# Kernel tuning notes

Measured on AMD Instinct MI355X. Metric: run time of the kernel, lower is better.

The kernel has to match this reference:

```python
import jax, jax.numpy as jnp
import numpy as np

SEQ_DIM = 256
PAIR_DIM = 128
N_HEADS = 8
HIDDEN = 32
B, L = 4, 512


def layer_norm(x, gamma, beta, eps=1e-5):
    mu = jnp.mean(x, axis=-1, keepdims=True)
    var = jnp.var(x, axis=-1, keepdims=True)
    return (x - mu) * jax.lax.rsqrt(var + eps) * gamma + beta


def setup_inputs() -> dict:
    key = jax.random.key(0)
    ks = jax.random.split(key, 12)
    d = N_HEADS * HIDDEN
    s = 0.02
    return {
        "seq": jax.random.normal(ks[0], (B, L, SEQ_DIM), jnp.float32),
        "pair": jax.random.normal(ks[1], (B, L, L, PAIR_DIM), jnp.float32),
        "ln_seq_g": jnp.ones((SEQ_DIM,), jnp.float32),
        "ln_seq_b": jnp.zeros((SEQ_DIM,), jnp.float32),
        "ln_pair_g": jnp.ones((PAIR_DIM,), jnp.float32),
        "ln_pair_b": jnp.zeros((PAIR_DIM,), jnp.float32),
        "W_b": jax.random.normal(ks[2], (PAIR_DIM, N_HEADS), jnp.float32) * s,
        "W_q": jax.random.normal(ks[3], (SEQ_DIM, d), jnp.float32) * s,
        "W_k": jax.random.normal(ks[4], (SEQ_DIM, d), jnp.float32) * s,
        "W_v": jax.random.normal(ks[5], (SEQ_DIM, d), jnp.float32) * s,
        "W_g": jax.random.normal(ks[6], (SEQ_DIM, d), jnp.float32) * s,
        "b_g": jnp.zeros((d,), jnp.float32),
        "W_o": jax.random.normal(ks[7], (d, SEQ_DIM), jnp.float32) * s,
        "b_o": jnp.zeros((SEQ_DIM,), jnp.float32),
    }


def reference(seq, pair, ln_seq_g, ln_seq_b, ln_pair_g, ln_pair_b,
              W_b, W_q, W_k, W_v, W_g, b_g, W_o, b_o):
    b, l, _ = seq.shape
    factor = 1.0 / np.sqrt(HIDDEN).astype(np.float32)
    s = layer_norm(seq, ln_seq_g, ln_seq_b)
    p = layer_norm(pair, ln_pair_g, ln_pair_b)
    Q = (s @ W_q).reshape(b, l, N_HEADS, HIDDEN)
    K = (s @ W_k).reshape(b, l, N_HEADS, HIDDEN)
    V = (s @ W_v).reshape(b, l, N_HEADS, HIDDEN)
    # pair bias: [b, i, j, n] -> [b, n, i, j]
    bias = jnp.einsum('bijp,pn->bnij', p, W_b)
    att = jnp.einsum('binh,bjnh->bnij', Q, K) * factor + bias
    att = jax.nn.softmax(att, axis=-1)
    gate = jax.nn.sigmoid(s @ W_g + b_g).reshape(b, l, N_HEADS, HIDDEN)
    out = jnp.einsum('bnij,bjnh->binh', att, V) * gate
    out = out.reshape(b, l, N_HEADS * HIDDEN)
    return out @ W_o + b_o
```

## Files before the change

kernel.cpp:

```cpp
#include <hip/hip_runtime.h>
#include <math.h>

#define OFF_Q    0
#define OFF_K    (524288)
#define OFF_V    (524288*2)
#define OFF_G    (524288*3)
#define OFF_PRE  (524288*4)
#define OFF_BIAS (524288*5)

template <int CTRL>
__device__ __forceinline__ float dpp_mov(float x) {
  return __int_as_float(__builtin_amdgcn_update_dpp(0, __float_as_int(x), CTRL, 0xF, 0xF, true));
}
template <int CTRL>
__device__ __forceinline__ float dpp_add(float x) { return x + dpp_mov<CTRL>(x); }
__device__ __forceinline__ float red16(float v) {
  v = dpp_add<0xB1>(v);
  v = dpp_add<0x4E>(v);
  v = dpp_add<0x141>(v);
  v = dpp_add<0x140>(v);
  return v;
}

#define SEL8(a, f, out) do { \
// ... 91 lines not shown
#pragma unroll 4
    for (int p = 0; p < 256; ++p) {
      float4 a  = *(const float4*)(ap + p*36);
      float4 bv = *(const float4*)(bp + p*256);
      a0.x = fmaf(a.x, bv.x, a0.x); a0.y = fmaf(a.x, bv.y, a0.y);
      a0.z = fmaf(a.x, bv.z, a0.z); a0.w = fmaf(a.x, bv.w, a0.w);
      a1.x = fmaf(a.y, bv.x, a1.x); a1.y = fmaf(a.y, bv.y, a1.y);
      a1.z = fmaf(a.y, bv.z, a1.z); a1.w = fmaf(a.y, bv.w, a1.w);
      a2.x = fmaf(a.z, bv.x, a2.x); a2.y = fmaf(a.z, bv.y, a2.y);
      a2.z = fmaf(a.z, bv.z, a2.z); a2.w = fmaf(a.z, bv.w, a2.w);
      a3.x = fmaf(a.w, bv.x, a3.x); a3.y = fmaf(a.w, bv.y, a3.y);
      a3.z = fmaf(a.w, bv.z, a3.z); a3.w = fmaf(a.w, bv.w, a3.w);
    }
    int mat = y >> 1;
    int col = cb + 4*cg2;
    float* outp = (mat == 0) ? Qw : (mat == 1) ? Kw : (mat == 2) ? Vw : Gw;
    if (mat == 0) {
      const float qs = 0.17677669529663687f;
      a0.x*=qs; a0.y*=qs; a0.z*=qs; a0.w*=qs;
      a1.x*=qs; a1.y*=qs; a1.z*=qs; a1.w*=qs;
      a2.x*=qs; a2.y*=qs; a2.z*=qs; a2.w*=qs;
      a3.x*=qs; a3.y*=qs; a3.z*=qs; a3.w*=qs;
    }
    if (mat == 3) {
      float4 g4 = *(const float4*)(bg + col);
      a0.x = 1.f/(1.f+__expf(-(a0.x+g4.x))); a0.y = 1.f/(1.f+__expf(-(a0.y+g4.y)));
      a0.z = 1.f/(1.f+__expf(-(a0.z+g4.z))); a0.w = 1.f/(1.f+__expf(-(a0.w+g4.w)));
      a1.x = 1.f/(1.f+__expf(-(a1.x+g4.x))); a1.y = 1.f/(1.f+__expf(-(a1.y+g4.y)));
      a1.z = 1.f/(1.f+__expf(-(a1.z+g4.z))); a1.w = 1.f/(1.f+__expf(-(a1.w+g4.w)));
      a2.x = 1.f/(1.f+__expf(-(a2.x+g4.x))); a2.y = 1.f/(1.f+__expf(-(a2.y+g4.y)));
      a2.z = 1.f/(1.f+__expf(-(a2.z+g4.z))); a2.w = 1.f/(1.f+__expf(-(a2.w+g4.w)));
      a3.x = 1.f/(1.f+__expf(-(a3.x+g4.x))); a3.y = 1.f/(1.f+__expf(-(a3.y+g4.y)));
      a3.z = 1.f/(1.f+__expf(-(a3.z+g4.z))); a3.w = 1.f/(1.f+__expf(-(a3.w+g4.w)));
    }
    int orow = m0 + 4*rg;
    *(float4*)(outp + (size_t)(orow+0)*256 + col) = a0;
    *(float4*)(outp + (size_t)(orow+1)*256 + col) = a1;
    *(float4*)(outp + (size_t)(orow+2)*256 + col) = a2;
    *(float4*)(outp + (size_t)(orow+3)*256 + col) = a3;
    return;
  }

  int bb2 = blk - 512;
  int b = bb2 >> 9, i = bb2 & 511;
  int lane = t & 63, w = t >> 6;
  int grp = lane >> 4, f = lane & 15;

  float wp[64];
  float cg[8] = {0,0,0,0,0,0,0,0}, cbv[8] = {0,0,0,0,0,0,0,0};
#pragma unroll
  for (int q = 0; q < 4; ++q) {
    int kA = 4*f + q, kB = 64 + 4*f + q;
    float gA = lpg[kA], bA = lpb[kA];
    float gB = lpg[kB], bB = lpb[kB];
    float4 uA0 = *(const float4*)(Wb + kA*8);
    float4 uA1 = *(const float4*)(Wb + kA*8 + 4);
    float4 uB0 = *(const float4*)(Wb + kB*8);
    float4 uB1 = *(const float4*)(Wb + kB*8 + 4);
    wp[q*8+0] = gA*uA0.x; cg[0] += wp[q*8+0]; cbv[0] = fmaf(bA, uA0.x, cbv[0]);
    wp[q*8+1] = gA*uA0.y; cg[1] += wp[q*8+1]; cbv[1] = fmaf(bA, uA0.y, cbv[1]);
    wp[q*8+2] = gA*uA0.z; cg[2] += wp[q*8+2]; cbv[2] = fmaf(bA, uA0.z, cbv[2]);
    wp[q*8+3] = gA*uA0.w; cg[3] += wp[q*8+3]; cbv[3] = fmaf(bA, uA0.w, cbv[3]);
    wp[q*8+4] = gA*uA1.x; cg[4] += wp[q*8+4]; cbv[4] = fmaf(bA, uA1.x, cbv[4]);
    wp[q*8+5] = gA*uA1.y; cg[5] += wp[q*8+5]; cbv[5] = fmaf(bA, uA1.y, cbv[5]);
    wp[q*8+6] = gA*uA1.z; cg[6] += wp[q*8+6]; cbv[6] = fmaf(bA, uA1.z, cbv[6]);
    wp[q*8+7] = gA*uA1.w; cg[7] += wp[q*8+7]; cbv[7] = fmaf(bA, uA1.w, cbv[7]);
    int qb8 = (4+q)*8;
    wp[qb8+0] = gB*uB0.x; cg[0] += wp[qb8+0]; cbv[0] = fmaf(bB, uB0.x, cbv[0]);
    wp[qb8+1] = gB*uB0.y; cg[1] += wp[qb8+1]; cbv[1] = fmaf(bB, uB0.y, cbv[1]);
    wp[qb8+2] = gB*uB0.z; cg[2] += wp[qb8+2]; cbv[2] = fmaf(bB, uB0.z, cbv[2]);
    wp[qb8+3] = gB*uB0.w; cg[3] += wp[qb8+3]; cbv[3] = fmaf(bB, uB0.w, cbv[3]);
    wp[qb8+4] = gB*uB1.x; cg[4] += wp[qb8+4]; cbv[4] = fmaf(bB, uB1.x, cbv[4]);
    wp[qb8+5] = gB*uB1.y; cg[5] += wp[qb8+5]; cbv[5] = fmaf(bB, uB1.y, cbv[5]);
    wp[qb8+6] = gB*uB1.z; cg[6] += wp[qb8+6]; cbv[6] = fmaf(bB, uB1.z, cbv[6]);
    wp[qb8+7] = gB*uB1.w; cg[7] += wp[qb8+7]; cbv[7] = fmaf(bB, uB1.w, cbv[7]);
  }
#pragma unroll
  for (int n2 = 0; n2 < 8; ++n2) { cg[n2] = red16(cg[n2]); cbv[n2] = red16(cbv[n2]); }
  float cgsel, cbsel;
  SEL8(cg, f, cgsel);
  SEL8(cbv, f, cbsel);

  const float* prow0 = pair + (size_t)(b*512 + i) * (512*128);
  float* bw0 = biasw + (size_t)(b*8)*262144 + (size_t)i*512;

  int j = 4*w + grp;
  const float* rp = prow0 + (size_t)j*128 + 4*f;
  float4 x0 = *(const float4*)rp;
  float4 x1 = *(const float4*)(rp + 64);
#pragma unroll 2
  for (int it = 0; it < 32; ++it) {
    float4 y0, y1;
    if (it < 31) {
      const float* rn = rp + 16*128;
      y0 = *(const float4*)rn;
      y1 = *(const float4*)(rn + 64);
    }
    float s  = x0.x + x0.y + x0.z + x0.w + x1.x + x1.y + x1.z + x1.w;
    float sq = x0.x*x0.x;
    sq = fmaf(x0.y, x0.y, sq); sq = fmaf(x0.z, x0.z, sq); sq = fmaf(x0.w, x0.w, sq);
    sq = fmaf(x1.x, x1.x, sq); sq = fmaf(x1.y, x1.y, sq);
    sq = fmaf(x1.z, x1.z, sq); sq = fmaf(x1.w, x1.w, sq);
    float dd[8];
#pragma unroll
    for (int n2 = 0; n2 < 8; ++n2) {
      float d = x0.x * wp[n2];
      d = fmaf(x0.y, wp[8+n2],  d);
      d = fmaf(x0.z, wp[16+n2], d);
      d = fmaf(x0.w, wp[24+n2], d);
      d = fmaf(x1.x, wp[32+n2], d);
      d = fmaf(x1.y, wp[40+n2], d);
      d = fmaf(x1.z, wp[48+n2], d);
      d = fmaf(x1.w, wp[56+n2], d);
      dd[n2] = d;
    }
    s  = red16(s);
    sq = red16(sq);
#pragma unroll
    for (int n2 = 0; n2 < 8; ++n2) dd[n2] = red16(dd[n2]);
    float mu = s * (1.f/128.f);
    float var = fmaf(sq, 1.f/128.f, -mu*mu);
    float rstd = rsqrtf(var + 1e-5f);
    if (f < 8) {
      float dv;
      SEL8(dd, f, dv);
      bw0[(size_t)f*262144 + j] = fmaf(rstd, fmaf(-mu, cgsel, dv), cbsel);
    }
    j += 16; rp += 16*128;
    x0 = y0; x1 = y1;
  }
}

#define KVS 260
#define BBS 36

__global__ __launch_bounds__(512, 2) void k_attn2(
    const float* __restrict__ Qw, const float* __restrict__ Kw, const float* __restrict__ Vw,
    const float* __restrict__ Gw, const float* __restrict__ biasw, float* __restrict__ prew) {
  __shared__ __align__(16) float Kb[2][32*KVS];
  __shared__ __align__(16) float Vb[2][32*KVS];
  __shared__ __align__(16) float Bb[2][64*BBS];
  __shared__ __align__(16) float scr[4*8*68];

  int t = threadIdx.x, lane = t & 63, w = t >> 6;
  int b = blockIdx.x >> 6, i0 = (blockIdx.x & 63) << 3;
  int n = lane >> 3, js = lane & 7;
  int ip = w & 3, jset = w >> 2;
  int ila = 2*ip, ilb = ila + 1;
  size_t qra = (size_t)(b*512 + i0 + ila);
  size_t qrb = qra + 1;

  float4 qa[8], qb[8];
  {
    const float* pa = Qw + qra*256 + n*32;
    const float* pb = Qw + qrb*256 + n*32;
#pragma unroll
    for (int x = 0; x < 8; ++x) { qa[x] = *(const float4*)(pa + 4*x); qb[x] = *(const float4*)(pb + 4*x); }
  }
  float4 acca[8], accb[8];
#pragma unroll
  for (int x = 0; x < 8; ++x) { acca[x] = make_float4(0,0,0,0); accb[x] = make_float4(0,0,0,0); }
  float ma = -1e30f, la = 0.f, mb2 = -1e30f, lb2 = 0.f;

  const float* Kg = Kw + (size_t)(b*512)*256;
  const float* Vg = Vw + (size_t)(b*512)*256;
  int sidx = 8*w + (lane >> 3);
  int s_il = sidx >> 3, s_n = sidx & 7;
  const float* bgsrc = biasw + (size_t)((b*8 + s_n)*512 + i0 + s_il)*512 + 4*(lane & 7);

  float4 sk[4], sv[4], sb;

#define STAGE_LOAD(tn) { \
    const float* ks_ = Kg + (size_t)((tn)*32 + 4*w)*256 + 4*lane; \
    const float* vs_ = Vg + (size_t)((tn)*32 + 4*w)*256 + 4*lane; \
    sk[0] = *(const float4*)(ks_);        sk[1] = *(const float4*)(ks_ + 256); \
    sk[2] = *(const float4*)(ks_ + 512);  sk[3] = *(const float4*)(ks_ + 768); \
    sv[0] = *(const float4*)(vs_);        sv[1] = *(const float4*)(vs_ + 256); \
    sv[2] = *(const float4*)(vs_ + 512);  sv[3] = *(const float4*)(vs_ + 768); \
    sb = *(const float4*)(bgsrc + (tn)*32); \
  }
#define STAGE_WRITE(tn) { int bf_ = (tn) & 1; \
    float* kd_ = &Kb[bf_][(4*w)*KVS + 4*lane]; \
    *(float4*)(kd_)         = sk[0]; *(float4*)(kd_ + KVS)   = sk[1]; \
    *(float4*)(kd_ + 2*KVS) = sk[2]; *(float4*)(kd_ + 3*KVS) = sk[3]; \
    float* vd_ = &Vb[bf_][(4*w)*KVS + 4*lane]; \
    *(float4*)(vd_)         = sv[0]; *(float4*)(vd_ + KVS)   = sv[1]; \
    *(float4*)(vd_ + 2*KVS) = sv[2]; *(float4*)(vd_ + 3*KVS) = sv[3]; \
    *(float4*)(&Bb[bf_][sidx*BBS + 4*(lane & 7)]) = sb; \
  }

  STAGE_LOAD(0);
  STAGE_WRITE(0);
  __syncthreads();

  int jl0 = jset*16 + js;
  for (int tt = 0; tt < 16; ++tt) {
    int cur = tt & 1;
    if (tt < 15) STAGE_LOAD(tt+1);

    const float* Kt = Kb[cur];
    const float* Vt = Vb[cur];
    const float* Bt = Bb[cur];

    float lga0, lga1, lgb0, lgb1;
    {
      const float* kp = Kt + jl0*KVS + n*32;
      float da = 0.f, db = 0.f;
#pragma unroll
      for (int x = 0; x < 8; ++x) {
        float4 kk = *(const float4*)(kp + 4*x);
        da = dot4(qa[x], kk, da); db = dot4(qb[x], kk, db);
      }
      lga0 = da + Bt[(ila*8 + n)*BBS + jl0];
      lgb0 = db + Bt[(ilb*8 + n)*BBS + jl0];
    }
    {
      const float* kp = Kt + (jl0+8)*KVS + n*32;
      float da = 0.f, db = 0.f;
#pragma unroll
      for (int x = 0; x < 8; ++x) {
        float4 kk = *(const float4*)(kp + 4*x);
        da = dot4(qa[x], kk, da); db = dot4(qb[x], kk, db);
      }
      lga1 = da + Bt[(ila*8 + n)*BBS + jl0 + 8];
      lgb1 = db + Bt[(ilb*8 + n)*BBS + jl0 + 8];
    }
    {
      float tm = fmaxf(lga0, lga1);
      float M = fmaxf(ma, tm);
      float sc = __expf(ma - M);
      la *= sc;
#pragma unroll
      for (int x = 0; x < 8; ++x) {
        acca[x].x *= sc; acca[x].y *= sc; acca[x].z *= sc; acca[x].w *= sc;
      }
      ma = M;
    }
    {
      float tm = fmaxf(lgb0, lgb1);
      float M = fmaxf(mb2, tm);
      float sc = __expf(mb2 - M);
      lb2 *= sc;
#pragma unroll
      for (int x = 0; x < 8; ++x) {
        accb[x].x *= sc; accb[x].y *= sc; accb[x].z *= sc; accb[x].w *= sc;
      }
      mb2 = M;
    }
    float pa0 = __expf(lga0 - ma), pa1 = __expf(lga1 - ma);
    float pb0 = __expf(lgb0 - mb2), pb1 = __expf(lgb1 - mb2);
    la += pa0 + pa1; lb2 += pb0 + pb1;
    {
      const float* vp = Vt + jl0*KVS + n*32;
#pragma unroll
      for (int x = 0; x < 8; ++x) {
        float4 vv = *(const float4*)(vp + 4*x);
        acca[x].x = fmaf(pa0, vv.x, acca[x].x); acca[x].y = fmaf(pa0, vv.y, acca[x].y);
        acca[x].z = fmaf(pa0, vv.z, acca[x].z); acca[x].w = fmaf(pa0, vv.w, acca[x].w);
        accb[x].x = fmaf(pb0, vv.x, accb[x].x); accb[x].y = fmaf(pb0, vv.y, accb[x].y);
        accb[x].z = fmaf(pb0, vv.z, accb[x].z); accb[x].w = fmaf(pb0, vv.w, accb[x].w);
      }
    }
    {
      const float* vp = Vt + (jl0+8)*KVS + n*32;
#pragma unroll
      for (int x = 0; x < 8; ++x) {
        float4 vv = *(const float4*)(vp + 4*x);
        acca[x].x = fmaf(pa1, vv.x, acca[x].x); acca[x].y = fmaf(pa1, vv.y, acca[x].y);
        acca[x].z = fmaf(pa1, vv.z, acca[x].z); acca[x].w = fmaf(pa1, vv.w, acca[x].w);
        accb[x].x = fmaf(pb1, vv.x, accb[x].x); accb[x].y = fmaf(pb1, vv.y, accb[x].y);
        accb[x].z = fmaf(pb1, vv.z, accb[x].z); accb[x].w = fmaf(pb1, vv.w, accb[x].w);
      }
    }

    if (tt < 15) STAGE_WRITE(tt+1);
    __syncthreads();
  }

  merge_dpp<0xB1>(ma, la, acca);   merge_dpp<0xB1>(mb2, lb2, accb);
  merge_dpp<0x4E>(ma, la, acca);   merge_dpp<0x4E>(mb2, lb2, accb);
  merge_dpp<0x141>(ma, la, acca);  merge_dpp<0x141>(mb2, lb2, accb);

  float4 fa = sel8_f4(acca, js);
  float4 fb = sel8_f4(accb, js);

  if (jset == 1) {
    int base = (ip*8 + n)*68;
    *(float4*)(scr + base + 4*js) = fa;
    *(float4*)(scr + base + 32 + 4*js) = fb;
    if (js == 0) { scr[base+64] = ma; scr[base+65] = la; scr[base+66] = mb2; scr[base+67] = lb2; }
  }
  __syncthreads();
  if (jset == 0) {
    int base = (ip*8 + n)*68;
    float4 a2 = *(const float4*)(scr + base + 4*js);
    float4 b2 = *(const float4*)(scr + base + 32 + 4*js);
    float m2a = scr[base+64], l2a = scr[base+65];
    float m2b = scr[base+66], l2b = scr[base+67];
    {
      float M = fmaxf(ma, m2a);
      float ea = __expf(ma - M), eb = __expf(m2a - M);
      float inv = 1.f / (la*ea + l2a*eb);
      float4 g4 = *(const float4*)(Gw + qra*256 + n*32 + 4*js);
      float4 r;
      r.x = (fa.x*ea + a2.x*eb) * inv * g4.x;
      r.y = (fa.y*ea + a2.y*eb) * inv * g4.y;
      r.z = (fa.z*ea + a2.z*eb) * inv * g4.z;
      r.w = (fa.w*ea + a2.w*eb) * inv * g4.w;
      *(float4*)(prew + qra*256 + n*32 + 4*js) = r;
    }
    {
      float M = fmaxf(mb2, m2b);
      float ea = __expf(mb2 - M), eb = __expf(m2b - M);
      float inv = 1.f / (lb2*ea + l2b*eb);
      float4 g4 = *(const float4*)(Gw + qrb*256 + n*32 + 4*js);
      float4 r;
      r.x = (fb.x*ea + b2.x*eb) * inv * g4.x;
      r.y = (fb.y*ea + b2.y*eb) * inv * g4.y;
      r.z = (fb.z*ea + b2.z*eb) * inv * g4.z;
      r.w = (fb.w*ea + b2.w*eb) * inv * g4.w;
      *(float4*)(prew + qrb*256 + n*32 + 4*js) = r;
    }
  }
}

__global__ __launch_bounds__(256) void k_out(
    const float* __restrict__ prew, const float* __restrict__ Wo, const float* __restrict__ bo,
    float* __restrict__ out) {
  __shared__ __align__(16) float As[256*36];
  int t = threadIdx.x;
  int m0 = blockIdx.x * 32;
  int y = blockIdx.y;
  {
    int r = t >> 3, c0 = t & 7;
    const float* srow = prew + (size_t)(m0 + r)*256;
#pragma unroll
    for (int qq = 0; qq < 8; ++qq) {
      int c4 = c0 + 8*qq;
      float4 v = *(const float4*)(srow + 4*c4);
      float* dp = As + 4*c4*36 + r;
      dp[0] = v.x; dp[36] = v.y; dp[72] = v.z; dp[108] = v.w;
    }
  }
  __syncthreads();
  int cb = y*128;
  int rg = t >> 5, cg2 = t & 31;
  int col = cb + 4*cg2;
  const float* bp = Wo + col;
  const float* ap = As + 4*rg;
  float4 a0 = {0,0,0,0}, a1 = {0,0,0,0}, a2 = {0,0,0,0}, a3 = {0,0,0,0};
#pragma unroll 4
  for (int p = 0; p < 256; ++p) {
    float4 a  = *(const float4*)(ap + p*36);
    float4 bv = *(const float4*)(bp + p*256);
    a0.x = fmaf(a.x, bv.x, a0.x); a0.y = fmaf(a.x, bv.y, a0.y);
    a0.z = fmaf(a.x, bv.z, a0.z); a0.w = fmaf(a.x, bv.w, a0.w);
    a1.x = fmaf(a.y, bv.x, a1.x); a1.y = fmaf(a.y, bv.y, a1.y);
    a1.z = fmaf(a.y, bv.z, a1.z); a1.w = fmaf(a.y, bv.w, a1.w);
    a2.x = fmaf(a.z, bv.x, a2.x); a2.y = fmaf(a.z, bv.y, a2.y);
    a2.z = fmaf(a.z, bv.z, a2.z); a2.w = fmaf(a.z, bv.w, a2.w);
    a3.x = fmaf(a.w, bv.x, a3.x); a3.y = fmaf(a.w, bv.y, a3.y);
    a3.z = fmaf(a.w, bv.z, a3.z); a3.w = fmaf(a.w, bv.w, a3.w);
  }
  float4 b4 = *(const float4*)(bo + col);
  a0.x += b4.x; a0.y += b4.y; a0.z += b4.z; a0.w += b4.w;
  a1.x += b4.x; a1.y += b4.y; a1.z += b4.z; a1.w += b4.w;
  a2.x += b4.x; a2.y += b4.y; a2.z += b4.z; a2.w += b4.w;
  a3.x += b4.x; a3.y += b4.y; a3.z += b4.z; a3.w += b4.w;
  int orow = m0 + 4*rg;
  *(float4*)(out + (size_t)(orow+0)*256 + col) = a0;
  *(float4*)(out + (size_t)(orow+1)*256 + col) = a1;
  *(float4*)(out + (size_t)(orow+2)*256 + col) = a2;
  *(float4*)(out + (size_t)(orow+3)*256 + col) = a3;
}

extern "C" void kernel_launch(void* const* d_in, const int* in_sizes, int n_in,
                              void* d_out, int out_size, void* d_ws, size_t ws_size,
                              hipStream_t stream) {
  const float* seq  = (const float*)d_in[0];
  const float* pair = (const float*)d_in[1];
  const float* lsg  = (const float*)d_in[2];
  const float* lsb  = (const float*)d_in[3];
  const float* lpg  = (const float*)d_in[4];
  const float* lpb  = (const float*)d_in[5];
  const float* Wb   = (const float*)d_in[6];
  const float* Wq   = (const float*)d_in[7];
  const float* Wk   = (const float*)d_in[8];
  const float* Wv   = (const float*)d_in[9];
  const float* Wg   = (const float*)d_in[10];
  const float* bg   = (const float*)d_in[11];
  const float* Wo   = (const float*)d_in[12];
  const float* bo   = (const float*)d_in[13];
  float* ws   = (float*)d_ws;
  float* Qw   = ws + OFF_Q;
  float* Kw   = ws + OFF_K;
  float* Vw   = ws + OFF_V;
  float* Gw   = ws + OFF_G;
  float* prew = ws + OFF_PRE;
  float* biasw= ws + OFF_BIAS;
  float* out  = (float*)d_out;

  hipLaunchKernelGGL(k_mega, dim3(2560), dim3(256), 0, stream,
                     seq, lsg, lsb, lpg, lpb, Wb, Wq, Wk, Wv, Wg, bg, pair,
                     Qw, Kw, Vw, Gw, biasw);
  hipLaunchKernelGGL(k_attn2, dim3(256), dim3(512), 0, stream,
                     Qw, Kw, Vw, Gw, biasw, prew);
  hipLaunchKernelGGL(k_out, dim3(64, 2), dim3(256), 0, stream,
                     prew, Wo, bo, out);
}
```

Baseline: 242.5 us.

## Rewrite attention kernel to stream K/V from global without LDS staging

```diff
diff --git a/kernel.cpp b/kernel.cpp
--- a/kernel.cpp
+++ b/kernel.cpp
@@ -197,7 +197,7 @@
   SEL8(cbv, f, cbsel);
 
   const float* prow0 = pair + (size_t)(b*512 + i) * (512*128);
-  float* bw0 = biasw + (size_t)(b*8)*262144 + (size_t)i*512;
+  float* bw0 = biasw + (size_t)(b*512 + i) * 512 * 8;
 
   int j = 4*w + grp;
   const float* rp = prow0 + (size_t)j*128 + 4*f;
@@ -239,31 +239,24 @@
     if (f < 8) {
       float dv;
       SEL8(dd, f, dv);
-      bw0[(size_t)f*262144 + j] = fmaf(rstd, fmaf(-mu, cgsel, dv), cbsel);
+      bw0[(size_t)j*8 + f] = fmaf(rstd, fmaf(-mu, cgsel, dv), cbsel);
     }
     j += 16; rp += 16*128;
     x0 = y0; x1 = y1;
   }
 }
 
-#define KVS 260
-#define BBS 36
-
-__global__ __launch_bounds__(512, 2) void k_attn2(
+__global__ __launch_bounds__(256, 1) void k_attn3(
     const float* __restrict__ Qw, const float* __restrict__ Kw, const float* __restrict__ Vw,
     const float* __restrict__ Gw, const float* __restrict__ biasw, float* __restrict__ prew) {
-  __shared__ __align__(16) float Kb[2][32*KVS];
-  __shared__ __align__(16) float Vb[2][32*KVS];
-  __shared__ __align__(16) float Bb[2][64*BBS];
-  __shared__ __align__(16) float scr[4*8*68];
-
-  int t = threadIdx.x, lane = t & 63, w = t >> 6;
-  int b = blockIdx.x >> 6, i0 = (blockIdx.x & 63) << 3;
+  int t = threadIdx.x, lane = t & 63, wid = t >> 6;
+  int bid = blockIdx.x;
+  int b = (bid & 7) >> 1;
+  int q = ((bid >> 3) << 1) | (bid & 1);
+  int P = q*4 + wid;
+  int ia = 2*P;
+  size_t qra = (size_t)(b*512 + ia), qrb = qra + 1;
   int n = lane >> 3, js = lane & 7;
-  int ip = w & 3, jset = w >> 2;
-  int ila = 2*ip, ilb = ila + 1;
-  size_t qra = (size_t)(b*512 + i0 + ila);
-  size_t qrb = qra + 1;
 
   float4 qa[8], qb[8];
   {
@@ -275,167 +268,77 @@
   float4 acca[8], accb[8];
 #pragma unroll
   for (int x = 0; x < 8; ++x) { acca[x] = make_float4(0,0,0,0); accb[x] = make_float4(0,0,0,0); }
-  float ma = -1e30f, la = 0.f, mb2 = -1e30f, lb2 = 0.f;
-
-  const float* Kg = Kw + (size_t)(b*512)*256;
-  const float* Vg = Vw + (size_t)(b*512)*256;
-  int sidx = 8*w + (lane >> 3);
-  int s_il = sidx >> 3, s_n = sidx & 7;
-  const float* bgsrc = biasw + (size_t)((b*8 + s_n)*512 + i0 + s_il)*512 + 4*(lane & 7);
-
-  float4 sk[4], sv[4], sb;
-
-#define STAGE_LOAD(tn) { \
-    const float* ks_ = Kg + (size_t)((tn)*32 + 4*w)*256 + 4*lane; \
-    const float* vs_ = Vg + (size_t)((tn)*32 + 4*w)*256 + 4*lane; \
-    sk[0] = *(const float4*)(ks_);        sk[1] = *(const float4*)(ks_ + 256); \
-    sk[2] = *(const float4*)(ks_ + 512);  sk[3] = *(const float4*)(ks_ + 768); \
-    sv[0] = *(const float4*)(vs_);        sv[1] = *(const float4*)(vs_ + 256); \
-    sv[2] = *(const float4*)(vs_ + 512);  sv[3] = *(const float4*)(vs_ + 768); \
-    sb = *(const float4*)(bgsrc + (tn)*32); \
-  }
-#define STAGE_WRITE(tn) { int bf_ = (tn) & 1; \
-    float* kd_ = &Kb[bf_][(4*w)*KVS + 4*lane]; \
-    *(float4*)(kd_)         = sk[0]; *(float4*)(kd_ + KVS)   = sk[1]; \
-    *(float4*)(kd_ + 2*KVS) = sk[2]; *(float4*)(kd_ + 3*KVS) = sk[3]; \
-    float* vd_ = &Vb[bf_][(4*w)*KVS + 4*lane]; \
-    *(float4*)(vd_)         = sv[0]; *(float4*)(vd_ + KVS)   = sv[1]; \
-    *(float4*)(vd_ + 2*KVS) = sv[2]; *(float4*)(vd_ + 3*KVS) = sv[3]; \
-    *(float4*)(&Bb[bf_][sidx*BBS + 4*(lane & 7)]) = sb; \
-  }
-
-  STAGE_LOAD(0);
-  STAGE_WRITE(0);
-  __syncthreads();
-
-  int jl0 = jset*16 + js;
-  for (int tt = 0; tt < 16; ++tt) {
-    int cur = tt & 1;
-    if (tt < 15) STAGE_LOAD(tt+1);
-
-    const float* Kt = Kb[cur];
-    const float* Vt = Vb[cur];
-    const float* Bt = Bb[cur];
-
-    float lga0, lga1, lgb0, lgb1;
-    {
-      const float* kp = Kt + jl0*KVS + n*32;
-      float da = 0.f, db = 0.f;
-#pragma unroll
-      for (int x = 0; x < 8; ++x) {
-        float4 kk = *(const float4*)(kp + 4*x);
-        da = dot4(qa[x], kk, da); db = dot4(qb[x], kk, db);
-      }
-      lga0 = da + Bt[(ila*8 + n)*BBS + jl0];
-      lgb0 = db + Bt[(ilb*8 + n)*BBS + jl0];
-    }
-    {
-      const float* kp = Kt + (jl0+8)*KVS + n*32;
-      float da = 0.f, db = 0.f;
-#pragma unroll
-      for (int x = 0; x < 8; ++x) {
-        float4 kk = *(const float4*)(kp + 4*x);
-        da = dot4(qa[x], kk, da); db = dot4(qb[x], kk, db);
-      }
-      lga1 = da + Bt[(ila*8 + n)*BBS + jl0 + 8];
-      lgb1 = db + Bt[(ilb*8 + n)*BBS + jl0 + 8];
-    }
-    {
-      float tm = fmaxf(lga0, lga1);
-      float M = fmaxf(ma, tm);
-      float sc = __expf(ma - M);
+  float ma = -1e30f, la = 0.f, mb = -1e30f, lb = 0.f;
+
+  const float* kp = Kw + (size_t)(b*512 + js)*256 + n*32;
+  const float* vp = Vw + (size_t)(b*512 + js)*256 + n*32;
+  const float* Bpa = biasw + ((size_t)(b*512 + ia)*512)*8 + js*8 + n;
+  const float* Bpb = Bpa + 512*8;
+
+  for (int s = 0; s < 64; ++s) {
+    float4 kc[8], vc[8];
+#pragma unroll
+    for (int x = 0; x < 8; ++x) kc[x] = *(const float4*)(kp + 4*x);
+#pragma unroll
+    for (int x = 0; x < 8; ++x) vc[x] = *(const float4*)(vp + 4*x);
+    float bba = Bpa[s*64];
+    float bbb = Bpb[s*64];
+
+    float da = 0.f, db = 0.f;
+#pragma unroll
+    for (int x = 0; x < 8; ++x) { da = dot4(qa[x], kc[x], da); db = dot4(qb[x], kc[x], db); }
+    float lga = da + bba, lgb = db + bbb;
+
+    if (lga > ma) {
+      float sc = __expf(ma - lga);
       la *= sc;
 #pragma unroll
       for (int x = 0; x < 8; ++x) {
         acca[x].x *= sc; acca[x].y *= sc; acca[x].z *= sc; acca[x].w *= sc;
       }
-      ma = M;
-    }
-    {
-      float tm = fmaxf(lgb0, lgb1);
-      float M = fmaxf(mb2, tm);
-      float sc = __expf(mb2 - M);
-      lb2 *= sc;
+      ma = lga;
+    }
+    if (lgb > mb) {
+      float sc = __expf(mb - lgb);
+      lb *= sc;
 #pragma unroll
       for (int x = 0; x < 8; ++x) {
         accb[x].x *= sc; accb[x].y *= sc; accb[x].z *= sc; accb[x].w *= sc;
       }
-      mb2 = M;
-    }
-    float pa0 = __expf(lga0 - ma), pa1 = __expf(lga1 - ma);
-    float pb0 = __expf(lgb0 - mb2), pb1 = __expf(lgb1 - mb2);
-    la += pa0 + pa1; lb2 += pb0 + pb1;
-    {
-      const float* vp = Vt + jl0*KVS + n*32;
-#pragma unroll
-      for (int x = 0; x < 8; ++x) {
-        float4 vv = *(const float4*)(vp + 4*x);
-        acca[x].x = fmaf(pa0, vv.x, acca[x].x); acca[x].y = fmaf(pa0, vv.y, acca[x].y);
-        acca[x].z = fmaf(pa0, vv.z, acca[x].z); acca[x].w = fmaf(pa0, vv.w, acca[x].w);
-        accb[x].x = fmaf(pb0, vv.x, accb[x].x); accb[x].y = fmaf(pb0, vv.y, accb[x].y);
-        accb[x].z = fmaf(pb0, vv.z, accb[x].z); accb[x].w = fmaf(pb0, vv.w, accb[x].w);
-      }
-    }
-    {
-      const float* vp = Vt + (jl0+8)*KVS + n*32;
-#pragma unroll
-      for (int x = 0; x < 8; ++x) {
-        float4 vv = *(const float4*)(vp + 4*x);
-        acca[x].x = fmaf(pa1, vv.x, acca[x].x); acca[x].y = fmaf(pa1, vv.y, acca[x].y);
-        acca[x].z = fmaf(pa1, vv.z, acca[x].z); acca[x].w = fmaf(pa1, vv.w, acca[x].w);
-        accb[x].x = fmaf(pb1, vv.x, accb[x].x); accb[x].y = fmaf(pb1, vv.y, accb[x].y);
-        accb[x].z = fmaf(pb1, vv.z, accb[x].z); accb[x].w = fmaf(pb1, vv.w, accb[x].w);
-      }
-    }
-
-    if (tt < 15) STAGE_WRITE(tt+1);
-    __syncthreads();
-  }
-
-  merge_dpp<0xB1>(ma, la, acca);   merge_dpp<0xB1>(mb2, lb2, accb);
-  merge_dpp<0x4E>(ma, la, acca);   merge_dpp<0x4E>(mb2, lb2, accb);
-  merge_dpp<0x141>(ma, la, acca);  merge_dpp<0x141>(mb2, lb2, accb);
+      mb = lgb;
+    }
+    float pa_ = __expf(lga - ma), pb_ = __expf(lgb - mb);
+    la += pa_; lb += pb_;
+#pragma unroll
+    for (int x = 0; x < 8; ++x) {
+      acca[x].x = fmaf(pa_, vc[x].x, acca[x].x); acca[x].y = fmaf(pa_, vc[x].y, acca[x].y);
+      acca[x].z = fmaf(pa_, vc[x].z, acca[x].z); acca[x].w = fmaf(pa_, vc[x].w, acca[x].w);
+      accb[x].x = fmaf(pb_, vc[x].x, accb[x].x); accb[x].y = fmaf(pb_, vc[x].y, accb[x].y);
+      accb[x].z = fmaf(pb_, vc[x].z, accb[x].z); accb[x].w = fmaf(pb_, vc[x].w, accb[x].w);
+    }
+    kp += 8*256; vp += 8*256;
+  }
+
+  merge_dpp<0xB1>(ma, la, acca);   merge_dpp<0xB1>(mb, lb, accb);
+  merge_dpp<0x4E>(ma, la, acca);   merge_dpp<0x4E>(mb, lb, accb);
+  merge_dpp<0x141>(ma, la, acca);  merge_dpp<0x141>(mb, lb, accb);
 
   float4 fa = sel8_f4(acca, js);
   float4 fb = sel8_f4(accb, js);
-
-  if (jset == 1) {
-    int base = (ip*8 + n)*68;
-    *(float4*)(scr + base + 4*js) = fa;
-    *(float4*)(scr + base + 32 + 4*js) = fb;
-    if (js == 0) { scr[base+64] = ma; scr[base+65] = la; scr[base+66] = mb2; scr[base+67] = lb2; }
-  }
-  __syncthreads();
-  if (jset == 0) {
-    int base = (ip*8 + n)*68;
-    float4 a2 = *(const float4*)(scr + base + 4*js);
-    float4 b2 = *(const float4*)(scr + base + 32 + 4*js);
-    float m2a = scr[base+64], l2a = scr[base+65];
-    float m2b = scr[base+66], l2b = scr[base+67];
-    {
-      float M = fmaxf(ma, m2a);
-      float ea = __expf(ma - M), eb = __expf(m2a - M);
-      float inv = 1.f / (la*ea + l2a*eb);
-      float4 g4 = *(const float4*)(Gw + qra*256 + n*32 + 4*js);
-      float4 r;
-      r.x = (fa.x*ea + a2.x*eb) * inv * g4.x;
-      r.y = (fa.y*ea + a2.y*eb) * inv * g4.y;
-      r.z = (fa.z*ea + a2.z*eb) * inv * g4.z;
-      r.w = (fa.w*ea + a2.w*eb) * inv * g4.w;
-      *(float4*)(prew + qra*256 + n*32 + 4*js) = r;
-    }
-    {
-      float M = fmaxf(mb2, m2b);
-      float ea = __expf(mb2 - M), eb = __expf(m2b - M);
-      float inv = 1.f / (lb2*ea + l2b*eb);
-      float4 g4 = *(const float4*)(Gw + qrb*256 + n*32 + 4*js);
-      float4 r;
-      r.x = (fb.x*ea + b2.x*eb) * inv * g4.x;
-      r.y = (fb.y*ea + b2.y*eb) * inv * g4.y;
-      r.z = (fb.z*ea + b2.z*eb) * inv * g4.z;
-      r.w = (fb.w*ea + b2.w*eb) * inv * g4.w;
-      *(float4*)(prew + qrb*256 + n*32 + 4*js) = r;
-    }
+  float inva = 1.f / la, invb = 1.f / lb;
+  {
+    float4 g4 = *(const float4*)(Gw + qra*256 + n*32 + 4*js);
+    float4 r;
+    r.x = fa.x*inva*g4.x; r.y = fa.y*inva*g4.y;
+    r.z = fa.z*inva*g4.z; r.w = fa.w*inva*g4.w;
+    *(float4*)(prew + qra*256 + n*32 + 4*js) = r;
+  }
+  {
+    float4 g4 = *(const float4*)(Gw + qrb*256 + n*32 + 4*js);
+    float4 r;
+    r.x = fb.x*invb*g4.x; r.y = fb.y*invb*g4.y;
+    r.z = fb.z*invb*g4.z; r.w = fb.w*invb*g4.w;
+    *(float4*)(prew + qrb*256 + n*32 + 4*js) = r;
   }
 }
 
@@ -518,7 +421,7 @@
   hipLaunchKernelGGL(k_mega, dim3(2560), dim3(256), 0, stream,
                      seq, lsg, lsb, lpg, lpb, Wb, Wq, Wk, Wv, Wg, bg, pair,
                      Qw, Kw, Vw, Gw, biasw);
-  hipLaunchKernelGGL(k_attn2, dim3(256), dim3(512), 0, stream,
+  hipLaunchKernelGGL(k_attn3, dim3(256), dim3(256), 0, stream,
                      Qw, Kw, Vw, Gw, biasw, prew);
   hipLaunchKernelGGL(k_out, dim3(64, 2), dim3(256), 0, stream,
                      prew, Wo, bo, out);
```

Measured after the change: 291.9 us. 20.4% more time.

## Store pair bias head-innermost, read it directly, and single-buffer K/V in LDS

Applied to the files above, without the earlier changes.

```diff
diff --git a/kernel.cpp b/kernel.cpp
--- a/kernel.cpp
+++ b/kernel.cpp
@@ -197,65 +197,70 @@
   SEL8(cbv, f, cbsel);
 
   const float* prow0 = pair + (size_t)(b*512 + i) * (512*128);
-  float* bw0 = biasw + (size_t)(b*8)*262144 + (size_t)i*512;
+  float* bw0 = biasw + (size_t)(b*512 + i) * 512 * 8;
+
+#define PROCESS(X0, X1, JJ) { \
+    float s_  = X0.x + X0.y + X0.z + X0.w + X1.x + X1.y + X1.z + X1.w; \
+    float sq_ = X0.x*X0.x; \
+    sq_ = fmaf(X0.y, X0.y, sq_); sq_ = fmaf(X0.z, X0.z, sq_); sq_ = fmaf(X0.w, X0.w, sq_); \
+    sq_ = fmaf(X1.x, X1.x, sq_); sq_ = fmaf(X1.y, X1.y, sq_); \
+    sq_ = fmaf(X1.z, X1.z, sq_); sq_ = fmaf(X1.w, X1.w, sq_); \
+    float dd_[8]; \
+    _Pragma("unroll") \
+    for (int n2 = 0; n2 < 8; ++n2) { \
+      float d_ = X0.x * wp[n2]; \
+      d_ = fmaf(X0.y, wp[8+n2],  d_); \
+      d_ = fmaf(X0.z, wp[16+n2], d_); \
+      d_ = fmaf(X0.w, wp[24+n2], d_); \
+      d_ = fmaf(X1.x, wp[32+n2], d_); \
+      d_ = fmaf(X1.y, wp[40+n2], d_); \
+      d_ = fmaf(X1.z, wp[48+n2], d_); \
+      d_ = fmaf(X1.w, wp[56+n2], d_); \
+      dd_[n2] = d_; \
+    } \
+    s_  = red16(s_); \
+    sq_ = red16(sq_); \
+    _Pragma("unroll") \
+    for (int n2 = 0; n2 < 8; ++n2) dd_[n2] = red16(dd_[n2]); \
+    float mu_ = s_ * (1.f/128.f); \
+    float var_ = fmaf(sq_, 1.f/128.f, -mu_*mu_); \
+    float rstd_ = rsqrtf(var_ + 1e-5f); \
+    if (f < 8) { \
+      float dv_; \
+      SEL8(dd_, f, dv_); \
+      bw0[(size_t)(JJ)*8 + f] = fmaf(rstd_, fmaf(-mu_, cgsel, dv_), cbsel); \
+    } \
+  }
 
   int j = 4*w + grp;
   const float* rp = prow0 + (size_t)j*128 + 4*f;
-  float4 x0 = *(const float4*)rp;
-  float4 x1 = *(const float4*)(rp + 64);
-#pragma unroll 2
-  for (int it = 0; it < 32; ++it) {
-    float4 y0, y1;
-    if (it < 31) {
-      const float* rn = rp + 16*128;
-      y0 = *(const float4*)rn;
-      y1 = *(const float4*)(rn + 64);
-    }
-    float s  = x0.x + x0.y + x0.z + x0.w + x1.x + x1.y + x1.z + x1.w;
-    float sq = x0.x*x0.x;
-    sq = fmaf(x0.y, x0.y, sq); sq = fmaf(x0.z, x0.z, sq); sq = fmaf(x0.w, x0.w, sq);
-    sq = fmaf(x1.x, x1.x, sq); sq = fmaf(x1.y, x1.y, sq);
-    sq = fmaf(x1.z, x1.z, sq); sq = fmaf(x1.w, x1.w, sq);
-    float dd[8];
-#pragma unroll
-    for (int n2 = 0; n2 < 8; ++n2) {
-      float d = x0.x * wp[n2];
-      d = fmaf(x0.y, wp[8+n2],  d);
-      d = fmaf(x0.z, wp[16+n2], d);
-      d = fmaf(x0.w, wp[24+n2], d);
-      d = fmaf(x1.x, wp[32+n2], d);
-      d = fmaf(x1.y, wp[40+n2], d);
-      d = fmaf(x1.z, wp[48+n2], d);
-      d = fmaf(x1.w, wp[56+n2], d);
-      dd[n2] = d;
-    }
-    s  = red16(s);
-    sq = red16(sq);
-#pragma unroll
-    for (int n2 = 0; n2 < 8; ++n2) dd[n2] = red16(dd[n2]);
-    float mu = s * (1.f/128.f);
-    float var = fmaf(sq, 1.f/128.f, -mu*mu);
-    float rstd = rsqrtf(var + 1e-5f);
-    if (f < 8) {
-      float dv;
-      SEL8(dd, f, dv);
-      bw0[(size_t)f*262144 + j] = fmaf(rstd, fmaf(-mu, cgsel, dv), cbsel);
-    }
-    j += 16; rp += 16*128;
-    x0 = y0; x1 = y1;
-  }
-}
-
-#define KVS 260
-#define BBS 36
-
-__global__ __launch_bounds__(512, 2) void k_attn2(
+  float4 xA0 = *(const float4*)rp;
+  float4 xA1 = *(const float4*)(rp + 64);
+  float4 xB0 = *(const float4*)(rp + 16*128);
+  float4 xB1 = *(const float4*)(rp + 16*128 + 64);
+  for (int it = 0; it < 32; it += 2) {
+    int adv = (it + 2 < 32) ? 1 : 0;
+    const float* rnA = rp + (size_t)adv*32*128;
+    const float* rnB = rp + (size_t)adv*48*128;
+    float4 nA0 = *(const float4*)rnA;
+    float4 nA1 = *(const float4*)(rnA + 64);
+    float4 nB0 = *(const float4*)rnB;
+    float4 nB1 = *(const float4*)(rnB + 64);
+    PROCESS(xA0, xA1, j);
+    PROCESS(xB0, xB1, j + 16);
+    xA0 = nA0; xA1 = nA1; xB0 = nB0; xB1 = nB1;
+    j += 32; rp += 32*128;
+  }
+#undef PROCESS
+}
+
+__global__ __launch_bounds__(512) void k_attn4(
     const float* __restrict__ Qw, const float* __restrict__ Kw, const float* __restrict__ Vw,
     const float* __restrict__ Gw, const float* __restrict__ biasw, float* __restrict__ prew) {
-  __shared__ __align__(16) float Kb[2][32*KVS];
-  __shared__ __align__(16) float Vb[2][32*KVS];
-  __shared__ __align__(16) float Bb[2][64*BBS];
-  __shared__ __align__(16) float scr[4*8*68];
+  __shared__ __align__(16) float smem[18688];
+  float* Kl = smem;
+  float* Vl = smem + 9344;
+  float* scr = smem;
 
   int t = threadIdx.x, lane = t & 63, w = t >> 6;
   int b = blockIdx.x >> 6, i0 = (blockIdx.x & 63) << 3;
@@ -264,6 +269,7 @@
   int ila = 2*ip, ilb = ila + 1;
   size_t qra = (size_t)(b*512 + i0 + ila);
   size_t qrb = qra + 1;
+  int jl0 = jset*16 + js;
 
   float4 qa[8], qb[8];
   {
@@ -279,94 +285,88 @@
 
   const float* Kg = Kw + (size_t)(b*512)*256;
   const float* Vg = Vw + (size_t)(b*512)*256;
-  int sidx = 8*w + (lane >> 3);
-  int s_il = sidx >> 3, s_n = sidx & 7;
-  const float* bgsrc = biasw + (size_t)((b*8 + s_n)*512 + i0 + s_il)*512 + 4*(lane & 7);
-
-  float4 sk[4], sv[4], sb;
-
-#define STAGE_LOAD(tn) { \
-    const float* ks_ = Kg + (size_t)((tn)*32 + 4*w)*256 + 4*lane; \
-    const float* vs_ = Vg + (size_t)((tn)*32 + 4*w)*256 + 4*lane; \
-    sk[0] = *(const float4*)(ks_);        sk[1] = *(const float4*)(ks_ + 256); \
-    sk[2] = *(const float4*)(ks_ + 512);  sk[3] = *(const float4*)(ks_ + 768); \
-    sv[0] = *(const float4*)(vs_);        sv[1] = *(const float4*)(vs_ + 256); \
-    sv[2] = *(const float4*)(vs_ + 512);  sv[3] = *(const float4*)(vs_ + 768); \
-    sb = *(const float4*)(bgsrc + (tn)*32); \
-  }
-#define STAGE_WRITE(tn) { int bf_ = (tn) & 1; \
-    float* kd_ = &Kb[bf_][(4*w)*KVS + 4*lane]; \
-    *(float4*)(kd_)         = sk[0]; *(float4*)(kd_ + KVS)   = sk[1]; \
-    *(float4*)(kd_ + 2*KVS) = sk[2]; *(float4*)(kd_ + 3*KVS) = sk[3]; \
-    float* vd_ = &Vb[bf_][(4*w)*KVS + 4*lane]; \
-    *(float4*)(vd_)         = sv[0]; *(float4*)(vd_ + KVS)   = sv[1]; \
-    *(float4*)(vd_ + 2*KVS) = sv[2]; *(float4*)(vd_ + 3*KVS) = sv[3]; \
-    *(float4*)(&Bb[bf_][sidx*BBS + 4*(lane & 7)]) = sb; \
-  }
-
-  STAGE_LOAD(0);
-  STAGE_WRITE(0);
+  const float* Bpa = biasw + ((size_t)(b*512 + i0 + ila)*512 + jl0)*8 + n;
+  const float* Bpb = Bpa + 512*8;
+
+  float4 sk[4], sv[4];
+  int woff = (lane >> 3)*36 + (lane & 7)*4;
+
+#define SLOAD(tn) { \
+    const float* ks_ = Kg + ((size_t)(tn)*32 + 4*w)*256 + 4*lane; \
+    const float* vs_ = Vg + ((size_t)(tn)*32 + 4*w)*256 + 4*lane; \
+    sk[0] = *(const float4*)(ks_);       sk[1] = *(const float4*)(ks_ + 256); \
+    sk[2] = *(const float4*)(ks_ + 512); sk[3] = *(const float4*)(ks_ + 768); \
+    sv[0] = *(const float4*)(vs_);       sv[1] = *(const float4*)(vs_ + 256); \
+    sv[2] = *(const float4*)(vs_ + 512); sv[3] = *(const float4*)(vs_ + 768); \
+  }
+#define SWRITE() { \
+    float* kd_ = Kl + (4*w)*292 + woff; \
+    *(float4*)(kd_)       = sk[0]; *(float4*)(kd_ + 292) = sk[1]; \
+    *(float4*)(kd_ + 584) = sk[2]; *(float4*)(kd_ + 876) = sk[3]; \
+    float* vd_ = Vl + (4*w)*292 + woff; \
+    *(float4*)(vd_)       = sv[0]; *(float4*)(vd_ + 292) = sv[1]; \
+    *(float4*)(vd_ + 584) = sv[2]; *(float4*)(vd_ + 876) = sv[3]; \
+  }
+
+  SLOAD(0);
+  SWRITE();
   __syncthreads();
 
-  int jl0 = jset*16 + js;
   for (int tt = 0; tt < 16; ++tt) {
-    int cur = tt & 1;
-    if (tt < 15) STAGE_LOAD(tt+1);
-
-    const float* Kt = Kb[cur];
-    const float* Vt = Vb[cur];
-    const float* Bt = Bb[cur];
+    if (tt < 15) SLOAD(tt+1);
+    float bba0 = Bpa[tt*256], bba1 = Bpa[tt*256 + 64];
+    float bbb0 = Bpb[tt*256], bbb1 = Bpb[tt*256 + 64];
 
     float lga0, lga1, lgb0, lgb1;
     {
-      const float* kp = Kt + jl0*KVS + n*32;
+      const float* kp = Kl + jl0*292 + n*36;
       float da = 0.f, db = 0.f;
 #pragma unroll
       for (int x = 0; x < 8; ++x) {
         float4 kk = *(const float4*)(kp + 4*x);
         da = dot4(qa[x], kk, da); db = dot4(qb[x], kk, db);
       }
-      lga0 = da + Bt[(ila*8 + n)*BBS + jl0];
-      lgb0 = db + Bt[(ilb*8 + n)*BBS + jl0];
-    }
-    {
-      const float* kp = Kt + (jl0+8)*KVS + n*32;
+      lga0 = da + bba0; lgb0 = db + bbb0;
+    }
+    {
+      const float* kp = Kl + (jl0+8)*292 + n*36;
       float da = 0.f, db = 0.f;
 #pragma unroll
       for (int x = 0; x < 8; ++x) {
         float4 kk = *(const float4*)(kp + 4*x);
         da = dot4(qa[x], kk, da); db = dot4(qb[x], kk, db);
       }
-      lga1 = da + Bt[(ila*8 + n)*BBS + jl0 + 8];
-      lgb1 = db + Bt[(ilb*8 + n)*BBS + jl0 + 8];
+      lga1 = da + bba1; lgb1 = db + bbb1;
     }
     {
       float tm = fmaxf(lga0, lga1);
-      float M = fmaxf(ma, tm);
-      float sc = __expf(ma - M);
-      la *= sc;
-#pragma unroll
-      for (int x = 0; x < 8; ++x) {
-        acca[x].x *= sc; acca[x].y *= sc; acca[x].z *= sc; acca[x].w *= sc;
-      }
-      ma = M;
+      if (tm > ma) {
+        float sc = __expf(ma - tm);
+        la *= sc;
+#pragma unroll
+        for (int x = 0; x < 8; ++x) {
+          acca[x].x *= sc; acca[x].y *= sc; acca[x].z *= sc; acca[x].w *= sc;
+        }
+        ma = tm;
+      }
     }
     {
       float tm = fmaxf(lgb0, lgb1);
-      float M = fmaxf(mb2, tm);
-      float sc = __expf(mb2 - M);
-      lb2 *= sc;
-#pragma unroll
-      for (int x = 0; x < 8; ++x) {
-        accb[x].x *= sc; accb[x].y *= sc; accb[x].z *= sc; accb[x].w *= sc;
-      }
-      mb2 = M;
+      if (tm > mb2) {
+        float sc = __expf(mb2 - tm);
+        lb2 *= sc;
+#pragma unroll
+        for (int x = 0; x < 8; ++x) {
+          accb[x].x *= sc; accb[x].y *= sc; accb[x].z *= sc; accb[x].w *= sc;
+        }
+        mb2 = tm;
+      }
     }
     float pa0 = __expf(lga0 - ma), pa1 = __expf(lga1 - ma);
     float pb0 = __expf(lgb0 - mb2), pb1 = __expf(lgb1 - mb2);
     la += pa0 + pa1; lb2 += pb0 + pb1;
     {
-      const float* vp = Vt + jl0*KVS + n*32;
+      const float* vp = Vl + jl0*292 + n*36;
 #pragma unroll
       for (int x = 0; x < 8; ++x) {
         float4 vv = *(const float4*)(vp + 4*x);
@@ -377,7 +377,7 @@
       }
     }
     {
-      const float* vp = Vt + (jl0+8)*KVS + n*32;
+      const float* vp = Vl + (jl0+8)*292 + n*36;
 #pragma unroll
       for (int x = 0; x < 8; ++x) {
         float4 vv = *(const float4*)(vp + 4*x);
@@ -387,10 +387,14 @@
         accb[x].z = fmaf(pb1, vv.z, accb[x].z); accb[x].w = fmaf(pb1, vv.w, accb[x].w);
       }
     }
-
-    if (tt < 15) STAGE_WRITE(tt+1);
     __syncthreads();
-  }
+    if (tt < 15) {
+      SWRITE();
+      __syncthreads();
+    }
+  }
+#undef SLOAD
+#undef SWRITE
 
   merge_dpp<0xB1>(ma, la, acca);   merge_dpp<0xB1>(mb2, lb2, accb);
   merge_dpp<0x4E>(ma, la, acca);   merge_dpp<0x4E>(mb2, lb2, accb);
@@ -518,7 +522,7 @@
   hipLaunchKernelGGL(k_mega, dim3(2560), dim3(256), 0, stream,
                      seq, lsg, lsb, lpg, lpb, Wb, Wq, Wk, Wv, Wg, bg, pair,
                      Qw, Kw, Vw, Gw, biasw);
-  hipLaunchKernelGGL(k_attn2, dim3(256), dim3(512), 0, stream,
+  hipLaunchKernelGGL(k_attn4, dim3(256), dim3(512), 0, stream,
                      Qw, Kw, Vw, Gw, biasw, prew);
   hipLaunchKernelGGL(k_out, dim3(64, 2), dim3(256), 0, stream,
                      prew, Wo, bo, out);
```

Result: slower. 274.2 us (+13.1%).

## Store pair bias head-innermost and read it directly in attention kernel

Applied to the files above, without the earlier changes.

```diff
diff --git a/kernel.cpp b/kernel.cpp
--- a/kernel.cpp
+++ b/kernel.cpp
@@ -197,7 +197,7 @@
   SEL8(cbv, f, cbsel);
 
   const float* prow0 = pair + (size_t)(b*512 + i) * (512*128);
-  float* bw0 = biasw + (size_t)(b*8)*262144 + (size_t)i*512;
+  float* bw0 = biasw + (size_t)(b*512 + i) * 512 * 8;
 
   int j = 4*w + grp;
   const float* rp = prow0 + (size_t)j*128 + 4*f;
@@ -239,23 +239,19 @@
     if (f < 8) {
       float dv;
       SEL8(dd, f, dv);
-      bw0[(size_t)f*262144 + j] = fmaf(rstd, fmaf(-mu, cgsel, dv), cbsel);
+      bw0[(size_t)j*8 + f] = fmaf(rstd, fmaf(-mu, cgsel, dv), cbsel);
     }
     j += 16; rp += 16*128;
     x0 = y0; x1 = y1;
   }
 }
 
-#define KVS 260
-#define BBS 36
-
-__global__ __launch_bounds__(512, 2) void k_attn2(
+__global__ __launch_bounds__(512) void k_attn5(
     const float* __restrict__ Qw, const float* __restrict__ Kw, const float* __restrict__ Vw,
     const float* __restrict__ Gw, const float* __restrict__ biasw, float* __restrict__ prew) {
-  __shared__ __align__(16) float Kb[2][32*KVS];
-  __shared__ __align__(16) float Vb[2][32*KVS];
-  __shared__ __align__(16) float Bb[2][64*BBS];
-  __shared__ __align__(16) float scr[4*8*68];
+  __shared__ __align__(16) float Kb[2][32*292];
+  __shared__ __align__(16) float Vb[2][32*292];
+  float* scr = &Kb[0][0];
 
   int t = threadIdx.x, lane = t & 63, w = t >> 6;
   int b = blockIdx.x >> 6, i0 = (blockIdx.x & 63) << 3;
@@ -264,6 +260,7 @@
   int ila = 2*ip, ilb = ila + 1;
   size_t qra = (size_t)(b*512 + i0 + ila);
   size_t qrb = qra + 1;
+  int jl0 = jset*16 + js;
 
   float4 qa[8], qb[8];
   {
@@ -279,94 +276,92 @@
 
   const float* Kg = Kw + (size_t)(b*512)*256;
   const float* Vg = Vw + (size_t)(b*512)*256;
-  int sidx = 8*w + (lane >> 3);
-  int s_il = sidx >> 3, s_n = sidx & 7;
-  const float* bgsrc = biasw + (size_t)((b*8 + s_n)*512 + i0 + s_il)*512 + 4*(lane & 7);
-
-  float4 sk[4], sv[4], sb;
-
-#define STAGE_LOAD(tn) { \
-    const float* ks_ = Kg + (size_t)((tn)*32 + 4*w)*256 + 4*lane; \
-    const float* vs_ = Vg + (size_t)((tn)*32 + 4*w)*256 + 4*lane; \
-    sk[0] = *(const float4*)(ks_);        sk[1] = *(const float4*)(ks_ + 256); \
-    sk[2] = *(const float4*)(ks_ + 512);  sk[3] = *(const float4*)(ks_ + 768); \
-    sv[0] = *(const float4*)(vs_);        sv[1] = *(const float4*)(vs_ + 256); \
-    sv[2] = *(const float4*)(vs_ + 512);  sv[3] = *(const float4*)(vs_ + 768); \
-    sb = *(const float4*)(bgsrc + (tn)*32); \
-  }
-#define STAGE_WRITE(tn) { int bf_ = (tn) & 1; \
-    float* kd_ = &Kb[bf_][(4*w)*KVS + 4*lane]; \
-    *(float4*)(kd_)         = sk[0]; *(float4*)(kd_ + KVS)   = sk[1]; \
-    *(float4*)(kd_ + 2*KVS) = sk[2]; *(float4*)(kd_ + 3*KVS) = sk[3]; \
-    float* vd_ = &Vb[bf_][(4*w)*KVS + 4*lane]; \
-    *(float4*)(vd_)         = sv[0]; *(float4*)(vd_ + KVS)   = sv[1]; \
-    *(float4*)(vd_ + 2*KVS) = sv[2]; *(float4*)(vd_ + 3*KVS) = sv[3]; \
-    *(float4*)(&Bb[bf_][sidx*BBS + 4*(lane & 7)]) = sb; \
-  }
-
-  STAGE_LOAD(0);
-  STAGE_WRITE(0);
+  const float* Bpa = biasw + ((size_t)(b*512 + i0 + ila)*512 + jl0)*8 + n;
+  const float* Bpb = Bpa + 512*8;
+
+  float4 sk[4], sv[4];
+  int woff = (lane >> 3)*36 + (lane & 7)*4;
+
+#define SLOAD(tn) { \
+    const float* ks_ = Kg + ((size_t)(tn)*32 + 4*w)*256 + 4*lane; \
+    const float* vs_ = Vg + ((size_t)(tn)*32 + 4*w)*256 + 4*lane; \
+    sk[0] = *(const float4*)(ks_);       sk[1] = *(const float4*)(ks_ + 256); \
+    sk[2] = *(const float4*)(ks_ + 512); sk[3] = *(const float4*)(ks_ + 768); \
+    sv[0] = *(const float4*)(vs_);       sv[1] = *(const float4*)(vs_ + 256); \
+    sv[2] = *(const float4*)(vs_ + 512); sv[3] = *(const float4*)(vs_ + 768); \
+  }
+#define SWRITE(tn) { int bf_ = (tn) & 1; \
+    float* kd_ = &Kb[bf_][(4*w)*292 + woff]; \
+    *(float4*)(kd_)       = sk[0]; *(float4*)(kd_ + 292) = sk[1]; \
+    *(float4*)(kd_ + 584) = sk[2]; *(float4*)(kd_ + 876) = sk[3]; \
+    float* vd_ = &Vb[bf_][(4*w)*292 + woff]; \
+    *(float4*)(vd_)       = sv[0]; *(float4*)(vd_ + 292) = sv[1]; \
+    *(float4*)(vd_ + 584) = sv[2]; *(float4*)(vd_ + 876) = sv[3]; \
+  }
+
+  SLOAD(0);
+  SWRITE(0);
   __syncthreads();
 
-  int jl0 = jset*16 + js;
   for (int tt = 0; tt < 16; ++tt) {
     int cur = tt & 1;
-    if (tt < 15) STAGE_LOAD(tt+1);
+    if (tt < 15) SLOAD(tt+1);
 
     const float* Kt = Kb[cur];
     const float* Vt = Vb[cur];
-    const float* Bt = Bb[cur];
+    float bba0 = Bpa[tt*256], bba1 = Bpa[tt*256 + 64];
+    float bbb0 = Bpb[tt*256], bbb1 = Bpb[tt*256 + 64];
 
     float lga0, lga1, lgb0, lgb1;
     {
-      const float* kp = Kt + jl0*KVS + n*32;
+      const float* kp = Kt + jl0*292 + n*36;
       float da = 0.f, db = 0.f;
 #pragma unroll
       for (int x = 0; x < 8; ++x) {
         float4 kk = *(const float4*)(kp + 4*x);
         da = dot4(qa[x], kk, da); db = dot4(qb[x], kk, db);
       }
-      lga0 = da + Bt[(ila*8 + n)*BBS + jl0];
-      lgb0 = db + Bt[(ilb*8 + n)*BBS + jl0];
-    }
-    {
-      const float* kp = Kt + (jl0+8)*KVS + n*32;
+      lga0 = da + bba0; lgb0 = db + bbb0;
+    }
+    {
+      const float* kp = Kt + (jl0+8)*292 + n*36;
       float da = 0.f, db = 0.f;
 #pragma unroll
       for (int x = 0; x < 8; ++x) {
         float4 kk = *(const float4*)(kp + 4*x);
         da = dot4(qa[x], kk, da); db = dot4(qb[x], kk, db);
       }
-      lga1 = da + Bt[(ila*8 + n)*BBS + jl0 + 8];
-      lgb1 = db + Bt[(ilb*8 + n)*BBS + jl0 + 8];
+      lga1 = da + bba1; lgb1 = db + bbb1;
     }
     {
       float tm = fmaxf(lga0, lga1);
-      float M = fmaxf(ma, tm);
-      float sc = __expf(ma - M);
-      la *= sc;
-#pragma unroll
-      for (int x = 0; x < 8; ++x) {
-        acca[x].x *= sc; acca[x].y *= sc; acca[x].z *= sc; acca[x].w *= sc;
-      }
-      ma = M;
+      if (tm > ma) {
+        float sc = __expf(ma - tm);
+        la *= sc;
+#pragma unroll
+        for (int x = 0; x < 8; ++x) {
+          acca[x].x *= sc; acca[x].y *= sc; acca[x].z *= sc; acca[x].w *= sc;
+        }
+        ma = tm;
+      }
     }
     {
       float tm = fmaxf(lgb0, lgb1);
-      float M = fmaxf(mb2, tm);
-      float sc = __expf(mb2 - M);
-      lb2 *= sc;
-#pragma unroll
-      for (int x = 0; x < 8; ++x) {
-        accb[x].x *= sc; accb[x].y *= sc; accb[x].z *= sc; accb[x].w *= sc;
-      }
-      mb2 = M;
+      if (tm > mb2) {
+        float sc = __expf(mb2 - tm);
+        lb2 *= sc;
+#pragma unroll
+        for (int x = 0; x < 8; ++x) {
+          accb[x].x *= sc; accb[x].y *= sc; accb[x].z *= sc; accb[x].w *= sc;
+        }
+        mb2 = tm;
+      }
     }
     float pa0 = __expf(lga0 - ma), pa1 = __expf(lga1 - ma);
     float pb0 = __expf(lgb0 - mb2), pb1 = __expf(lgb1 - mb2);
     la += pa0 + pa1; lb2 += pb0 + pb1;
     {
-      const float* vp = Vt + jl0*KVS + n*32;
+      const float* vp = Vt + jl0*292 + n*36;
 #pragma unroll
       for (int x = 0; x < 8; ++x) {
         float4 vv = *(const float4*)(vp + 4*x);
@@ -377,7 +372,7 @@
       }
     }
     {
-      const float* vp = Vt + (jl0+8)*KVS + n*32;
+      const float* vp = Vt + (jl0+8)*292 + n*36;
 #pragma unroll
       for (int x = 0; x < 8; ++x) {
         float4 vv = *(const float4*)(vp + 4*x);
@@ -388,9 +383,11 @@
       }
     }
 
-    if (tt < 15) STAGE_WRITE(tt+1);
+    if (tt < 15) SWRITE(tt+1);
     __syncthreads();
   }
+#undef SLOAD
+#undef SWRITE
 
   merge_dpp<0xB1>(ma, la, acca);   merge_dpp<0xB1>(mb2, lb2, accb);
   merge_dpp<0x4E>(ma, la, acca);   merge_dpp<0x4E>(mb2, lb2, accb);
@@ -518,7 +515,7 @@
   hipLaunchKernelGGL(k_mega, dim3(2560), dim3(256), 0, stream,
                      seq, lsg, lsb, lpg, lpb, Wb, Wq, Wk, Wv, Wg, bg, pair,
                      Qw, Kw, Vw, Gw, biasw);
-  hipLaunchKernelGGL(k_attn2, dim3(256), dim3(512), 0, stream,
+  hipLaunchKernelGGL(k_attn5, dim3(256), dim3(512), 0, stream,
                      Qw, Kw, Vw, Gw, biasw, prew);
   hipLaunchKernelGGL(k_out, dim3(64, 2), dim3(256), 0, stream,
                      prew, Wo, bo, out);
```

Result: faster. 211.1 us (-12.9%).
